# Optimization experiments

Hardware: AMD Instinct MI355X
Metric: run time of the kernel (lower is better)

Reference implementation:

```python
import jax, jax.numpy as jnp
import numpy as np

DENSE_W = 0.7  # unused in learned fusion path but kept for parity
SPARSE_W = 0.3

def _l2norm(x):
    return x / jnp.linalg.norm(x, axis=-1, keepdims=True)

def setup_inputs() -> dict:
    key = jax.random.key(0)
    ks = jax.random.split(key, 8)
    Q, D, dim = 32, 4096, 384
    feat = 2 * dim + 2  # 770
    query_dense = _l2norm(jax.random.normal(ks[0], (Q, dim), jnp.float32))
    doc_dense = _l2norm(jax.random.normal(ks[1], (D, dim), jnp.float32))
    sparse_scores = jax.random.uniform(ks[2], (Q, D), jnp.float32)
    W1 = jax.random.normal(ks[3], (feat, 384), jnp.float32) * (1.0 / np.sqrt(feat))
    b1 = jnp.zeros((384,), jnp.float32)
    W2 = jax.random.normal(ks[4], (384, 192), jnp.float32) * (1.0 / np.sqrt(384))
    b2 = jnp.zeros((192,), jnp.float32)
    W3 = jax.random.normal(ks[5], (192, 1), jnp.float32) * (1.0 / np.sqrt(192))
    b3 = jnp.zeros((1,), jnp.float32)
    return {"query_dense": query_dense, "doc_dense": doc_dense,
            "sparse_scores": sparse_scores,
            "W1": W1, "b1": b1, "W2": W2, "b2": b2, "W3": W3, "b3": b3}

def reference(query_dense, doc_dense, sparse_scores, W1, b1, W2, b2, W3, b3):
    # dense cosine similarity (inputs are L2-normalized): [Q, D]
    dense_scores = query_dense @ doc_dense.T
    Q, D = dense_scores.shape
    dim = query_dense.shape[1]
    # Vectorized equivalent of the per-pair gather+concat double loop:
    # feature[q, d] = [query_dense[q], doc_dense[d], dense[q,d], sparse[q,d]]
    qf = jnp.broadcast_to(query_dense[:, None, :], (Q, D, dim))
    df = jnp.broadcast_to(doc_dense[None, :, :], (Q, D, dim))
    features = jnp.concatenate(
        [qf, df, dense_scores[..., None], sparse_scores[..., None]], axis=-1)  # [Q, D, 2*dim+2]
    # 4-layer fusion MLP (Dropout is identity at inference)
    h = jax.nn.relu(features @ W1 + b1)
    h = jax.nn.relu(h @ W2 + b2)
    fusion_weights = jax.nn.sigmoid((h @ W3 + b3)[..., 0])  # [Q, D]
    final_scores = fusion_weights * dense_scores + (1.0 - fusion_weights) * sparse_scores
    return final_scores, dense_scores, sparse_scores
```

## Files before the change

### kernel.cpp

```cpp
#include <hip/hip_runtime.h>
#include <hip/hip_bf16.h>

typedef __attribute__((ext_vector_type(4))) float f32x4;
typedef __attribute__((ext_vector_type(8))) short bf16x8;

__device__ __forceinline__ short f2bf(float x){
    __hip_bfloat16 h = __float2bfloat16(x);
    return __builtin_bit_cast(short, h);
}
__device__ __forceinline__ float bf2f(short x){
    unsigned int u = ((unsigned int)(unsigned short)x) << 16;
    return __builtin_bit_cast(float, u);
}

__global__ __launch_bounds__(256)
void pre_kernel(const float* __restrict__ query, const float* __restrict__ doc,
                const float* __restrict__ sparse, const float* __restrict__ W1,
                const float* __restrict__ b1,
                float* __restrict__ out_dense, float* __restrict__ out_sparse,
                short* __restrict__ Bws, float* __restrict__ Aq){
    __shared__ float ldsq[32*388];
    __shared__ float ldsd[16*388];
    const int b = blockIdx.x, tid = threadIdx.x;

    if (b < 256){
        const int d0 = b*16;
        #pragma unroll
        for (int i=0;i<12;i++){ int idx = tid + i*256; int row = idx/96, c4 = idx%96;
            *(f32x4*)(ldsq + row*388 + c4*4) = *(const f32x4*)(query + row*384 + c4*4); }
        #pragma unroll
        for (int i=0;i<6;i++){ int idx = tid + i*256; int row = idx/96, c4 = idx%96;
            *(f32x4*)(ldsd + row*388 + c4*4) = *(const f32x4*)(doc + (d0+row)*384 + c4*4); }
        __syncthreads();
        const int q = tid>>3, dg = tid&7;
        float acc0 = 0.0f, acc1 = 0.0f;
        #pragma unroll 4
        for (int k=0;k<384;k++){
            float qv = ldsq[q*388 + k];
            acc0 += qv*ldsd[dg*388 + k];
            acc1 += qv*ldsd[(dg+8)*388 + k];
        }
        out_dense[q*4096 + d0 + dg]     = acc0;
        out_dense[q*4096 + d0 + dg + 8] = acc1;
        if (tid < 128){
            int qq = tid>>2, c4 = tid&3;
            *(f32x4*)(out_sparse + qq*4096 + d0 + c4*4) = *(const f32x4*)(sparse + qq*4096 + d0 + c4*4);
        }
    } else {
        const int bb = b - 256;
        const int w = tid >> 6, lane = tid & 63;
        const int cl = lane & 15, quad = lane >> 4;
        const float* src; const float* wrow; int r0; bool isA;
        if (bb < 256){ r0 = bb*16;       src = doc;   wrow = W1 + 384*384; isA = false; }
        else         { r0 = (bb-256)*16; src = query; wrow = W1;           isA = true;  }

        f32x4 acc[6];
        #pragma unroll
        for (int t=0;t<6;t++) acc[t] = (f32x4){0.f,0.f,0.f,0.f};

        #pragma unroll 1
        for (int s=0;s<12;s++){
            const float* ap = src + (r0+cl)*384 + s*32 + quad*8;
            const f32x4 a0 = *(const f32x4*)ap;
            const f32x4 a1 = *(const f32x4*)(ap+4);
            bf16x8 af;
            #pragma unroll
            for (int j=0;j<4;j++){ af[j] = f2bf(a0[j]); af[4+j] = f2bf(a1[j]); }
            const float* wk = wrow + (s*32 + quad*8)*384;
            #pragma unroll
            for (int tt=0;tt<6;tt++){
                const int col = (w*6+tt)*16 + cl;
                bf16x8 bf_;
                #pragma unroll
                for (int j=0;j<8;j++) bf_[j] = f2bf(wk[j*384 + col]);
                acc[tt] = __builtin_amdgcn_mfma_f32_16x16x32_bf16(af, bf_, acc[tt], 0, 0, 0);
            }
        }
        #pragma unroll
        for (int tt=0;tt<6;tt++){
            const int col = (w*6+tt)*16 + cl;
            if (isA){
                const float b1v = b1[col];
                #pragma unroll
                for (int r=0;r<4;r++)
                    Aq[(r0 + quad*4 + r)*384 + col] = acc[tt][r] + b1v;
            } else {
                #pragma unroll
                for (int r=0;r<4;r++)
                    Bws[(r0 + quad*4 + r)*384 + col] = f2bf(acc[tt][r]);
            }
        }
    }
}

__global__ __launch_bounds__(512, 2)
void main_kernel(const float* __restrict__ Aq, const short* __restrict__ Bws,
                 const float* __restrict__ W1, const float* __restrict__ W2,
                 const float* __restrict__ b2, const float* __restrict__ W3,
                 const float* __restrict__ b3, const float* __restrict__ sparse,
                 const float* __restrict__ dense_in, float* __restrict__ out_final){
    __shared__ short lw[73728];
    const int tid = threadIdx.x;
    #pragma unroll
    for (int i=0;i<18;i++){
        int c = tid + i*512;
        int lane_c = c & 63, st = c >> 6;
        int s = st/12, t = st%12;
        int n = t*16 + (lane_c&15), kb = s*32 + ((lane_c>>4)&3)*8;
        bf16x8 v;
        #pragma unroll
        for (int j=0;j<8;j++) v[j] = f2bf(W2[(kb+j)*192 + n]);
        *(bf16x8*)(lw + c*8) = v;
    }
    __syncthreads();

    const int lane = tid & 63, w = tid >> 6;
    const int cl = lane & 15, quad = lane >> 4;
    const int pair = w >> 1, h = w & 1;
    const int q = h*16 + cl;
    const float b3v = b3[0];
    const float* w1c = W1 + 768*384;
    const float* w1d = W1 + 769*384;

    #pragma unroll 1
    for (int t4=0; t4<4; t4++){
        const int dcol = blockIdx.x*16 + t4*4 + pair;
        const float dsv = dense_in[q*4096 + dcol];
        const float ssv = sparse[q*4096 + dcol];

        f32x4 acc[12];
        #pragma unroll
        for (int t=0;t<12;t++) acc[t] = (f32x4){0.f,0.f,0.f,0.f};

        bf16x8 bw_c = *(const bf16x8*)(Bws + dcol*384 + quad*8);
        f32x4  a0_c = *(const f32x4*)(Aq + q*384 + quad*8);
        f32x4  a1_c = *(const f32x4*)(Aq + q*384 + quad*8 + 4);

        #pragma unroll 1
        for (int s=0;s<12;s++){
            const int k0 = s*32 + quad*8;
            const int kn = (s < 11) ? (k0 + 32) : (quad*8);
            const bf16x8 bw_n = *(const bf16x8*)(Bws + dcol*384 + kn);
            const f32x4  a0_n = *(const f32x4*)(Aq + q*384 + kn);
            const f32x4  a1_n = *(const f32x4*)(Aq + q*384 + kn + 4);
            const f32x4 wc0 = *(const f32x4*)(w1c + k0);
            const f32x4 wc1 = *(const f32x4*)(w1c + k0 + 4);
            const f32x4 wd0 = *(const f32x4*)(w1d + k0);
            const f32x4 wd1 = *(const f32x4*)(w1d + k0 + 4);
            bf16x8 fr;
            #pragma unroll
            for (int j=0;j<4;j++){
                float h0 = a0_c[j] + bf2f(bw_c[j])   + dsv*wc0[j] + ssv*wd0[j];
                float h1 = a1_c[j] + bf2f(bw_c[4+j]) + dsv*wc1[j] + ssv*wd1[j];
                fr[j]   = f2bf(fmaxf(h0, 0.0f));
                fr[4+j] = f2bf(fmaxf(h1, 0.0f));
            }
            #pragma unroll
            for (int t=0;t<12;t++){
                const bf16x8 bfr = *(const bf16x8*)(lw + ((s*12 + t)*64 + lane)*8);
                acc[t] = __builtin_amdgcn_mfma_f32_16x16x32_bf16(fr, bfr, acc[t], 0, 0, 0);
            }
            bw_c = bw_n; a0_c = a0_n; a1_c = a1_n;
        }

        float p[4] = {0.f,0.f,0.f,0.f};
        #pragma unroll
        for (int t=0;t<12;t++){
            const float b2v = b2[t*16 + cl];
            const float w3v = W3[t*16 + cl];
            #pragma unroll
            for (int r=0;r<4;r++)
                p[r] += fmaxf(acc[t][r] + b2v, 0.0f) * w3v;
        }
        #pragma unroll
        for (int m=1; m<16; m<<=1){
            #pragma unroll
            for (int r=0;r<4;r++) p[r] += __shfl_xor(p[r], m);
        }
        if (cl == 0){
            #pragma unroll
            for (int r=0;r<4;r++){
                int qq = h*16 + quad*4 + r;
                float logit = p[r] + b3v;
                float wgt = 1.0f/(1.0f + __expf(-logit));
                float dd = dense_in[qq*4096 + dcol];
                float ss = sparse[qq*4096 + dcol];
                out_final[qq*4096 + dcol] = wgt*dd + (1.0f - wgt)*ss;
            }
        }
    }
}

extern "C" void kernel_launch(void* const* d_in, const int* in_sizes, int n_in,
                              void* d_out, int out_size, void* d_ws, size_t ws_size,
                              hipStream_t stream){
    const float* query  = (const float*)d_in[0];
    const float* doc    = (const float*)d_in[1];
    const float* sparse = (const float*)d_in[2];
    const float* W1     = (const float*)d_in[3];
    const float* b1     = (const float*)d_in[4];
    const float* W2     = (const float*)d_in[5];
    const float* b2     = (const float*)d_in[6];
    const float* W3     = (const float*)d_in[7];
    const float* b3     = (const float*)d_in[8];

    float* out_final  = (float*)d_out;
    float* out_dense  = (float*)d_out + 131072;
    float* out_sparse = (float*)d_out + 262144;

    short* Bws = (short*)d_ws;
    float* Aq  = (float*)((char*)d_ws + 3145728);

    hipLaunchKernelGGL(pre_kernel,  dim3(514), dim3(256), 0, stream,
                       query, doc, sparse, W1, b1, out_dense, out_sparse, Bws, Aq);
    hipLaunchKernelGGL(main_kernel, dim3(256), dim3(512), 0, stream,
                       Aq, Bws, W1, W2, b2, W3, b3, sparse, out_dense, out_final);
}
```

Baseline: 143.3 us.

## Switch main MLP to 32x32x16 MFMA and pre-pack W1 dense/sparse rows as bf16

The main kernel's second-layer GEMM now uses 32x32x16 bf16 MFMA tiles, with each wave covering all 32 queries for one document column, instead of 16x16x32 tiles split across wave pairs. The W2 LDS layout, the K loop (24 steps of 16) and the final reduction and sigmoid epilogue are rebuilt to match the 32x32 output layout. An extra pre_kernel block converts the two W1 rows that multiply the dense and sparse scores to bf16 in an interleaved layout, which cuts per-step global loads. The larger MFMA should reduce instruction count and LDS traffic per FLOP, at the cost of higher accumulator register pressure and a heavier cross-lane reduction.

```diff
diff --git a/kernel.cpp b/kernel.cpp
--- a/kernel.cpp
+++ b/kernel.cpp
@@ -1,8 +1,9 @@
 #include <hip/hip_runtime.h>
 #include <hip/hip_bf16.h>
 
-typedef __attribute__((ext_vector_type(4))) float f32x4;
-typedef __attribute__((ext_vector_type(8))) short bf16x8;
+typedef __attribute__((ext_vector_type(4)))  float f32x4;
+typedef __attribute__((ext_vector_type(16))) float f32x16;
+typedef __attribute__((ext_vector_type(8)))  short bf16x8;
 
 __device__ __forceinline__ short f2bf(float x){
     __hip_bfloat16 h = __float2bfloat16(x);
@@ -18,7 +19,7 @@
                 const float* __restrict__ sparse, const float* __restrict__ W1,
                 const float* __restrict__ b1,
                 float* __restrict__ out_dense, float* __restrict__ out_sparse,
-                short* __restrict__ Bws, float* __restrict__ Aq){
+                short* __restrict__ Bws, float* __restrict__ Aq, short* __restrict__ W1cd){
     __shared__ float ldsq[32*388];
     __shared__ float ldsd[16*388];
     const int b = blockIdx.x, tid = threadIdx.x;
@@ -46,7 +47,7 @@
             int qq = tid>>2, c4 = tid&3;
             *(f32x4*)(out_sparse + qq*4096 + d0 + c4*4) = *(const f32x4*)(sparse + qq*4096 + d0 + c4*4);
         }
-    } else {
+    } else if (b < 514){
         const int bb = b - 256;
         const int w = tid >> 6, lane = tid & 63;
         const int cl = lane & 15, quad = lane >> 4;
@@ -90,23 +91,32 @@
                     Bws[(r0 + quad*4 + r)*384 + col] = f2bf(acc[tt][r]);
             }
         }
+    } else {
+        #pragma unroll
+        for (int i=0;i<3;i++){
+            int o3 = tid + i*256;
+            int k = (o3>>4)*8 + (o3&7);
+            int which = (o3>>3)&1;
+            W1cd[o3] = f2bf(W1[(768+which)*384 + k]);
+        }
     }
 }
 
 __global__ __launch_bounds__(512, 2)
 void main_kernel(const float* __restrict__ Aq, const short* __restrict__ Bws,
-                 const float* __restrict__ W1, const float* __restrict__ W2,
+                 const short* __restrict__ W1cd,
                  const float* __restrict__ b2, const float* __restrict__ W3,
                  const float* __restrict__ b3, const float* __restrict__ sparse,
-                 const float* __restrict__ dense_in, float* __restrict__ out_final){
+                 const float* __restrict__ W2, const float* __restrict__ dense_in,
+                 float* __restrict__ out_final){
     __shared__ short lw[73728];
     const int tid = threadIdx.x;
     #pragma unroll
     for (int i=0;i<18;i++){
         int c = tid + i*512;
         int lane_c = c & 63, st = c >> 6;
-        int s = st/12, t = st%12;
-        int n = t*16 + (lane_c&15), kb = s*32 + ((lane_c>>4)&3)*8;
+        int s = st/6, t2 = st%6;
+        int n = t2*32 + (lane_c&31), kb = s*16 + ((lane_c>>5)&1)*8;
         bf16x8 v;
         #pragma unroll
         for (int j=0;j<8;j++) v[j] = f2bf(W2[(kb+j)*192 + n]);
@@ -115,78 +125,78 @@
     __syncthreads();
 
     const int lane = tid & 63, w = tid >> 6;
-    const int cl = lane & 15, quad = lane >> 4;
-    const int pair = w >> 1, h = w & 1;
-    const int q = h*16 + cl;
+    const int m = lane & 31, q2 = lane >> 5;
+    const int kbase = q2*8;
     const float b3v = b3[0];
-    const float* w1c = W1 + 768*384;
-    const float* w1d = W1 + 769*384;
 
     #pragma unroll 1
-    for (int t4=0; t4<4; t4++){
-        const int dcol = blockIdx.x*16 + t4*4 + pair;
-        const float dsv = dense_in[q*4096 + dcol];
-        const float ssv = sparse[q*4096 + dcol];
-
-        f32x4 acc[12];
-        #pragma unroll
-        for (int t=0;t<12;t++) acc[t] = (f32x4){0.f,0.f,0.f,0.f};
-
-        bf16x8 bw_c = *(const bf16x8*)(Bws + dcol*384 + quad*8);
-        f32x4  a0_c = *(const f32x4*)(Aq + q*384 + quad*8);
-        f32x4  a1_c = *(const f32x4*)(Aq + q*384 + quad*8 + 4);
+    for (int t4=0; t4<2; t4++){
+        const int dcol = blockIdx.x*16 + t4*8 + w;
+        const float dsv = dense_in[m*4096 + dcol];
+        const float ssv = sparse[m*4096 + dcol];
+
+        f32x16 acc[6];
+        #pragma unroll
+        for (int t=0;t<6;t++)
+            #pragma unroll
+            for (int r=0;r<16;r++) acc[t][r] = 0.0f;
+
+        bf16x8 bw_c = *(const bf16x8*)(Bws + dcol*384 + kbase);
+        f32x4  a0_c = *(const f32x4*)(Aq + m*384 + kbase);
+        f32x4  a1_c = *(const f32x4*)(Aq + m*384 + kbase + 4);
 
         #pragma unroll 1
-        for (int s=0;s<12;s++){
-            const int k0 = s*32 + quad*8;
-            const int kn = (s < 11) ? (k0 + 32) : (quad*8);
+        for (int s=0;s<24;s++){
+            const int k0 = s*16 + kbase;
+            const int kn = (s < 23) ? (k0 + 16) : kbase;
             const bf16x8 bw_n = *(const bf16x8*)(Bws + dcol*384 + kn);
-            const f32x4  a0_n = *(const f32x4*)(Aq + q*384 + kn);
-            const f32x4  a1_n = *(const f32x4*)(Aq + q*384 + kn + 4);
-            const f32x4 wc0 = *(const f32x4*)(w1c + k0);
-            const f32x4 wc1 = *(const f32x4*)(w1c + k0 + 4);
-            const f32x4 wd0 = *(const f32x4*)(w1d + k0);
-            const f32x4 wd1 = *(const f32x4*)(w1d + k0 + 4);
+            const f32x4  a0_n = *(const f32x4*)(Aq + m*384 + kn);
+            const f32x4  a1_n = *(const f32x4*)(Aq + m*384 + kn + 4);
+            const bf16x8 wcv = *(const bf16x8*)(W1cd + (s*2 + q2)*16);
+            const bf16x8 wdv = *(const bf16x8*)(W1cd + (s*2 + q2)*16 + 8);
             bf16x8 fr;
             #pragma unroll
             for (int j=0;j<4;j++){
-                float h0 = a0_c[j] + bf2f(bw_c[j])   + dsv*wc0[j] + ssv*wd0[j];
-                float h1 = a1_c[j] + bf2f(bw_c[4+j]) + dsv*wc1[j] + ssv*wd1[j];
+                float h0 = a0_c[j] + bf2f(bw_c[j])   + dsv*bf2f(wcv[j])   + ssv*bf2f(wdv[j]);
+                float h1 = a1_c[j] + bf2f(bw_c[4+j]) + dsv*bf2f(wcv[4+j]) + ssv*bf2f(wdv[4+j]);
                 fr[j]   = f2bf(fmaxf(h0, 0.0f));
                 fr[4+j] = f2bf(fmaxf(h1, 0.0f));
             }
             #pragma unroll
-            for (int t=0;t<12;t++){
-                const bf16x8 bfr = *(const bf16x8*)(lw + ((s*12 + t)*64 + lane)*8);
-                acc[t] = __builtin_amdgcn_mfma_f32_16x16x32_bf16(fr, bfr, acc[t], 0, 0, 0);
+            for (int t=0;t<6;t++){
+                const bf16x8 bfr = *(const bf16x8*)(lw + ((s*6 + t)*64 + lane)*8);
+                acc[t] = __builtin_amdgcn_mfma_f32_32x32x16_bf16(fr, bfr, acc[t], 0, 0, 0);
             }
             bw_c = bw_n; a0_c = a0_n; a1_c = a1_n;
         }
 
-        float p[4] = {0.f,0.f,0.f,0.f};
-        #pragma unroll
-        for (int t=0;t<12;t++){
-            const float b2v = b2[t*16 + cl];
-            const float w3v = W3[t*16 + cl];
-            #pragma unroll
-            for (int r=0;r<4;r++)
+        float p[16];
+        #pragma unroll
+        for (int r=0;r<16;r++) p[r] = 0.0f;
+        #pragma unroll
+        for (int t=0;t<6;t++){
+            const int n = t*32 + m;
+            const float b2v = b2[n];
+            const float w3v = W3[n];
+            #pragma unroll
+            for (int r=0;r<16;r++)
                 p[r] += fmaxf(acc[t][r] + b2v, 0.0f) * w3v;
         }
         #pragma unroll
-        for (int m=1; m<16; m<<=1){
-            #pragma unroll
-            for (int r=0;r<4;r++) p[r] += __shfl_xor(p[r], m);
-        }
-        if (cl == 0){
-            #pragma unroll
-            for (int r=0;r<4;r++){
-                int qq = h*16 + quad*4 + r;
-                float logit = p[r] + b3v;
-                float wgt = 1.0f/(1.0f + __expf(-logit));
-                float dd = dense_in[qq*4096 + dcol];
-                float ss = sparse[qq*4096 + dcol];
-                out_final[qq*4096 + dcol] = wgt*dd + (1.0f - wgt)*ss;
-            }
+        for (int mask=1; mask<32; mask<<=1){
+            #pragma unroll
+            for (int r=0;r<16;r++) p[r] += __shfl_xor(p[r], mask);
+        }
+        float myp = p[0];
+        #pragma unroll
+        for (int r=1;r<16;r++) myp = (m==r) ? p[r] : myp;
+        if (m < 16){
+            const int row = (m&3) + 8*(m>>2) + 4*q2;
+            float logit = myp + b3v;
+            float wgt = 1.0f/(1.0f + __expf(-logit));
+            float dd = dense_in[row*4096 + dcol];
+            float ss = sparse[row*4096 + dcol];
+            out_final[row*4096 + dcol] = wgt*dd + (1.0f - wgt)*ss;
         }
     }
 }
@@ -208,11 +218,12 @@
     float* out_dense  = (float*)d_out + 131072;
     float* out_sparse = (float*)d_out + 262144;
 
-    short* Bws = (short*)d_ws;
-    float* Aq  = (float*)((char*)d_ws + 3145728);
-
-    hipLaunchKernelGGL(pre_kernel,  dim3(514), dim3(256), 0, stream,
-                       query, doc, sparse, W1, b1, out_dense, out_sparse, Bws, Aq);
+    short* Bws  = (short*)d_ws;
+    float* Aq   = (float*)((char*)d_ws + 3145728);
+    short* W1cd = (short*)((char*)d_ws + 3194880);
+
+    hipLaunchKernelGGL(pre_kernel,  dim3(515), dim3(256), 0, stream,
+                       query, doc, sparse, W1, b1, out_dense, out_sparse, Bws, Aq, W1cd);
     hipLaunchKernelGGL(main_kernel, dim3(256), dim3(512), 0, stream,
-                       Aq, Bws, W1, W2, b2, W3, b3, sparse, out_dense, out_final);
-}
+                       Aq, Bws, W1cd, b2, W3, b3, sparse, W2, out_dense, out_final);
+}
```

Measured after the change: 136.4 us. 1.05x faster.
